# Optimization experiments

Hardware: AMD Instinct MI355X
Metric: run time of the kernel (lower is better)

## Reference

```python
import jax, jax.numpy as jnp
import numpy as np

N_EMBD = 512
N_HEADS = 8
N_KV_HEADS = 2
HEAD_DIM = N_EMBD // N_HEADS  # 64
ROPE_BASE = 1000000.0
B, T = 2, 4096


def _rotate_half(x):
    h = x.shape[-1] // 2
    return jnp.concatenate([-x[..., h:], x[..., :h]], axis=-1)


def _build_rope(head_dim, seq_len, base, dtype):
    inv_freq = 1.0 / base ** (jnp.arange(0, head_dim, 2, dtype=jnp.float32) / head_dim)
    t = jnp.arange(seq_len, dtype=jnp.float32)
    freqs = jnp.outer(t, inv_freq)            # [T, head_dim/2]
    emb = jnp.concatenate([freqs, freqs], axis=-1)  # [T, head_dim]
    return emb.astype(dtype), None  # placeholder, cos/sin computed by caller


def setup_inputs() -> dict:
    key = jax.random.key(0)
    ks = jax.random.split(key, 8)
    s_in = 1.0 / np.sqrt(N_EMBD)
    x = jax.random.normal(ks[0], (B, T, N_EMBD), dtype=jnp.float32)
    Wq = jax.random.normal(ks[1], (N_EMBD, N_HEADS * HEAD_DIM), dtype=jnp.float32) * s_in
    bq = jnp.zeros((N_HEADS * HEAD_DIM,), dtype=jnp.float32)
    Wk = jax.random.normal(ks[2], (N_EMBD, N_KV_HEADS * HEAD_DIM), dtype=jnp.float32) * s_in
    bk = jnp.zeros((N_KV_HEADS * HEAD_DIM,), dtype=jnp.float32)
    Wv = jax.random.normal(ks[3], (N_EMBD, N_KV_HEADS * HEAD_DIM), dtype=jnp.float32) * s_in
    bv = jnp.zeros((N_KV_HEADS * HEAD_DIM,), dtype=jnp.float32)
    Wo = jax.random.normal(ks[4], (N_HEADS * HEAD_DIM, N_EMBD), dtype=jnp.float32) * s_in
    return {"x": x, "Wq": Wq, "bq": bq, "Wk": Wk, "bk": bk, "Wv": Wv, "bv": bv, "Wo": Wo}


def reference(x, Wq, bq, Wk, bk, Wv, bv, Wo):
    Bx, Tx, _ = x.shape
    scale = HEAD_DIM ** -0.5
    q = (x @ Wq + bq).reshape(Bx, Tx, N_HEADS, HEAD_DIM).transpose(0, 2, 1, 3)      # [B,H,T,D]
    k = (x @ Wk + bk).reshape(Bx, Tx, N_KV_HEADS, HEAD_DIM).transpose(0, 2, 1, 3)   # [B,Hkv,T,D]
    v = (x @ Wv + bv).reshape(Bx, Tx, N_KV_HEADS, HEAD_DIM).transpose(0, 2, 1, 3)

    # RoPE (built in fp32 then cast, matching torch impl)
    inv_freq = 1.0 / ROPE_BASE ** (jnp.arange(0, HEAD_DIM, 2, dtype=jnp.float32) / HEAD_DIM)
    t = jnp.arange(Tx, dtype=jnp.float32)
    freqs = jnp.outer(t, inv_freq)
    emb = jnp.concatenate([freqs, freqs], axis=-1)          # [T, D]
    cos = jnp.cos(emb).astype(x.dtype)[None, None, :, :]    # broadcast over B,H
    sin = jnp.sin(emb).astype(x.dtype)[None, None, :, :]
    q = q * cos + _rotate_half(q) * sin
    k = k * cos + _rotate_half(k) * sin

    rep = N_HEADS // N_KV_HEADS
    k = jnp.repeat(k, rep, axis=1)   # repeat_interleave on head dim
    v = jnp.repeat(v, rep, axis=1)

    attn = jnp.einsum("bhtd,bhsd->bhts", q, k) * scale      # [B,H,T,T]
    causal = jnp.tril(jnp.ones((Tx, Tx), dtype=bool))
    attn = jnp.where(causal, attn, jnp.finfo(attn.dtype).min)
    attn = jax.nn.softmax(attn, axis=-1)
    out = jnp.einsum("bhts,bhsd->bhtd", attn, v)            # [B,H,T,D]
    out = out.transpose(0, 2, 1, 3).reshape(Bx, Tx, N_HEADS * HEAD_DIM)
    return out @ Wo
```

## Files before the change

kernel.cpp:

```cpp
#include <hip/hip_runtime.h>

typedef unsigned short u16;
typedef unsigned int u32;
typedef __bf16 bf16x8_t __attribute__((ext_vector_type(8)));
typedef float f32x4_t __attribute__((ext_vector_type(4)));
typedef float f32x16_t __attribute__((ext_vector_type(16)));

#define T_SEQ 4096
#define EMB 512
#define NH 8
#define NKV 2
#define HD 64

__device__ __forceinline__ float bf2f(u16 h) {
    union { unsigned u; float f; } x; x.u = ((unsigned)h) << 16; return x.f;
}
__device__ __forceinline__ u16 f2bf(float f) {
    union { float f; unsigned u; } x; x.f = f;
    unsigned r = x.u + 0x7FFFu + ((x.u >> 16) & 1u);
    return (u16)(r >> 16);
}

__global__ __launch_bounds__(256)
void prep_kernel(const float* __restrict__ x,
                 const float* __restrict__ Wq, const float* __restrict__ Wk,
                 const float* __restrict__ Wv, const float* __restrict__ Wo,
                 u16* __restrict__ WqkvT, u16* __restrict__ WoT,
                 u16* __restrict__ xbf, float* __restrict__ cost, float* __restrict__ sint)
{
    int i = blockIdx.x * 256 + threadIdx.x;
    if (i < 262144) {
        int n = i >> 9, k = i & 511;
        WqkvT[i] = f2bf(Wq[(size_t)k * 512 + n]);
    } else if (i < 327680) {
        int j = i - 262144;
        int n = j >> 9, k = j & 511;
        WqkvT[i] = f2bf(Wk[(size_t)k * 128 + n]);
    } else if (i < 393216) {
        int j = i - 327680;
        int n = j >> 9, k = j & 511;
        WqkvT[i] = f2bf(Wv[(size_t)k * 128 + n]);
    } else if (i < 655360) {
        int j = i - 393216;
        int n = j >> 9, k = j & 511;
        WoT[j] = f2bf(Wo[(size_t)k * 512 + n]);
    } else if (i < 1703936) {
        int j = i - 655360;
        float4 v = *reinterpret_cast<const float4*>(x + (size_t)j * 4);
        u16 o[4] = { f2bf(v.x), f2bf(v.y), f2bf(v.z), f2bf(v.w) };
        *reinterpret_cast<uint2*>(xbf + (size_t)j * 4) = *reinterpret_cast<uint2*>(o);
    } else {
        int j = i - 1703936;
        int t = j >> 5, jj = j & 31;
        double invf = pow(1.0e6, -(double)jj / 32.0);
        double ang = (double)t * invf;
        cost[j] = (float)cos(ang);
        sint[j] = (float)sin(ang);
    }
}

template <int EPI>
__global__ __launch_bounds__(256)
void gemm_kernel(const u16* __restrict__ A, const u16* __restrict__ Bt, int K,
                 float* __restrict__ C, int N,
                 const float* __restrict__ bq, const float* __restrict__ bk,
                 const float* __restrict__ bv,
                 const float* __restrict__ cost, const float* __restrict__ sint,
                 u16* __restrict__ qw, u16* __restrict__ kw, u16* __restrict__ vt)
{
    __shared__ __align__(16) u16 As[128][72];
    __shared__ __align__(16) u16 Bs[128][72];

    const int tid  = threadIdx.x;
    const int lane = tid & 63, wave = tid >> 6;
    const int wr = wave >> 1, wc = wave & 1;
    const int tm = blockIdx.x, tn = blockIdx.y;
    const int lrow = lane & 15, lgrp = lane >> 4;

    f32x4_t acc[4][4];
#pragma unroll
    for (int i = 0; i < 4; ++i)
#pragma unroll
        for (int j = 0; j < 4; ++j) acc[i][j] = (f32x4_t){0.f, 0.f, 0.f, 0.f};

    for (int k0 = 0; k0 < K; k0 += 64) {
        __syncthreads();
        {
            const int r0 = tid >> 3;
            const int ko = (tid & 7) * 8;
#pragma unroll
            for (int rr = 0; rr < 4; ++rr) {
                int row = r0 + rr * 32;
                uint4 va = *reinterpret_cast<const uint4*>(A + (size_t)(tm * 128 + row) * K + k0 + ko);
                *reinterpret_cast<uint4*>(&As[row][ko]) = va;
                uint4 vb = *reinterpret_cast<const uint4*>(Bt + (size_t)(tn * 128 + row) * K + k0 + ko);
                *reinterpret_cast<uint4*>(&Bs[row][ko]) = vb;
            }
        }
        __syncthreads();
#pragma unroll
        for (int kc = 0; kc < 2; ++kc) {
            bf16x8_t af[4], bf[4];
#pragma unroll
            for (int mb = 0; mb < 4; ++mb)
                af[mb] = *reinterpret_cast<const bf16x8_t*>(&As[wr * 64 + mb * 16 + lrow][kc * 32 + lgrp * 8]);
#pragma unroll
            for (int nb = 0; nb < 4; ++nb)
                bf[nb] = *reinterpret_cast<const bf16x8_t*>(&Bs[wc * 64 + nb * 16 + lrow][kc * 32 + lgrp * 8]);
#pragma unroll
            for (int mb = 0; mb < 4; ++mb)
#pragma unroll
                for (int nb = 0; nb < 4; ++nb)
                    acc[mb][nb] = __builtin_amdgcn_mfma_f32_16x16x32_bf16(af[mb], bf[nb], acc[mb][nb], 0, 0, 0);
        }
    }

    if (EPI == 0) {
#pragma unroll
        for (int mb = 0; mb < 4; ++mb)
#pragma unroll
            for (int nb = 0; nb < 4; ++nb)
#pragma unroll
                for (int r = 0; r < 4; ++r) {
                    int row = tm * 128 + wr * 64 + mb * 16 + lgrp * 4 + r;
                    int col = tn * 128 + wc * 64 + nb * 16 + lrow;
                    C[(size_t)row * N + col] = acc[mb][nb][r];
                }
    } else {
        const float QSC = 0.125f * 1.44269504088896f;
#pragma unroll
        for (int mb = 0; mb < 4; ++mb)
#pragma unroll
            for (int r = 0; r < 4; ++r) {
                int grow = tm * 128 + wr * 64 + mb * 16 + lgrp * 4 + r;
                int b = grow >> 12, t = grow & 4095;
#pragma unroll
                for (int nb = 0; nb < 2; ++nb) {
                    int n = tn * 128 + wc * 64 + nb * 16 + lrow;
                    int j = n & 63;
                    float c0 = acc[mb][nb][r];
                    float c1 = acc[mb][nb + 2][r];
                    if (n < 512) {
                        c0 += bq[n]; c1 += bq[n + 32];
                        float cs = cost[t * 32 + j], sn = sint[t * 32 + j];
                        float r0 = (c0 * cs - c1 * sn) * QSC;
                        float r1 = (c1 * cs + c0 * sn) * QSC;
                        int h = n >> 6;
                        size_t base = ((size_t)(b * NH + h) * T_SEQ + t) * HD;
                        qw[base + j]      = f2bf(r0);
                        qw[base + j + 32] = f2bf(r1);
                    } else if (n < 640) {
                        int nn = n - 512;
                        c0 += bk[nn]; c1 += bk[nn + 32];
                        float cs = cost[t * 32 + j], sn = sint[t * 32 + j];
                        float r0 = c0 * cs - c1 * sn;
                        float r1 = c1 * cs + c0 * sn;
                        int hk2 = nn >> 6;
                        size_t base = ((size_t)(b * NKV + hk2) * T_SEQ + t) * HD;
                        kw[base + j]      = f2bf(r0);
                        kw[base + j + 32] = f2bf(r1);
                    } else {
                        int nn = n - 640;
                        c0 += bv[nn]; c1 += bv[nn + 32];
                        int hv = nn >> 6;
                        size_t base = (size_t)(b * NKV + hv) * HD * T_SEQ;
                        vt[base + (size_t)j * T_SEQ + t]        = f2bf(c0);
                        vt[base + (size_t)(j + 32) * T_SEQ + t] = f2bf(c1);
                    }
                }
            }
    }
}

__global__ __launch_bounds__(256)
void attn_kernel(const u16* __restrict__ qw, const u16* __restrict__ kw,
                 const u16* __restrict__ vt, u16* __restrict__ po, float* __restrict__ lb)
{
    __shared__ __align__(16) u16 Ks[2][64][64];
    __shared__ __align__(16) u16 Vs[2][64][64];

    const int hdix = blockIdx.x;
    const int b = hdix >> 3, h = hdix & 7, hk = h >> 2;
    const int qt = 31 - (int)blockIdx.y;
    const int ck = blockIdx.z;
    const int tid = threadIdx.x, lane = tid & 63, wave = tid >> 6;
    const int lid = lane & 31, hi = lane >> 5;
    const int q0 = qt * 128 + wave * 32;
    const int kt0 = ck * (qt + 1);
    const int kt1 = kt0 + (qt + 1);

    const u16* kbase  = kw + (size_t)(b * NKV + hk) * T_SEQ * HD;
    const u16* vtbase = vt + (size_t)(b * NKV + hk) * HD * T_SEQ;

    const int ss = tid >> 3;
    const int sg = tid & 7;
    const int swz = (sg ^ (ss & 7)) << 3;

    bf16x8_t qf[4];
    {
        const u16* qrow = qw + ((size_t)(b * NH + h) * T_SEQ + q0 + lid) * HD + 8 * hi;
#pragma unroll
        for (int t = 0; t < 4; ++t)
            qf[t] = *reinterpret_cast<const bf16x8_t*>(qrow + 16 * t);
    }

    f32x16_t o0, o1, z16;
#pragma unroll
    for (int i = 0; i < 16; ++i) { o0[i] = 0.f; o1[i] = 0.f; z16[i] = 0.f; }
    const float M_FIX = 16.0f;
    float l = 0.f;

    {
        const int s2 = kt0 * 64;
        uint4 ka  = *reinterpret_cast<const uint4*>(kbase + (size_t)(s2 + ss) * HD + sg * 8);
        uint4 kb2 = *reinterpret_cast<const uint4*>(kbase + (size_t)(s2 + ss + 32) * HD + sg * 8);
        uint4 va  = *reinterpret_cast<const uint4*>(vtbase + (size_t)ss * T_SEQ + s2 + sg * 8);
        uint4 vb2 = *reinterpret_cast<const uint4*>(vtbase + (size_t)(ss + 32) * T_SEQ + s2 + sg * 8);
        *reinterpret_cast<uint4*>(&Ks[0][ss][swz]) = ka;
        *reinterpret_cast<uint4*>(&Ks[0][ss + 32][swz]) = kb2;
        *reinterpret_cast<uint4*>(&Vs[0][ss][swz]) = va;
        *reinterpret_cast<uint4*>(&Vs[0][ss + 32][swz]) = vb2;
    }
    __syncthreads();

    for (int kt = kt0; kt < kt1; ++kt) {
        const int cur = (kt - kt0) & 1, nxt = cur ^ 1;
        const bool pre = (kt + 1 < kt1);

        uint4 kr0, kr1, vr0, vr1;
        if (pre) {
            const int s2 = (kt + 1) * 64;
            kr0 = *reinterpret_cast<const uint4*>(kbase + (size_t)(s2 + ss) * HD + sg * 8);
            kr1 = *reinterpret_cast<const uint4*>(kbase + (size_t)(s2 + ss + 32) * HD + sg * 8);
            vr0 = *reinterpret_cast<const uint4*>(vtbase + (size_t)ss * T_SEQ + s2 + sg * 8);
            vr1 = *reinterpret_cast<const uint4*>(vtbase + (size_t)(ss + 32) * T_SEQ + s2 + sg * 8);
        }

        if (kt * 64 <= q0 + 31) {
            const bool full = (kt * 64 + 32 <= q0 + 31);
            const bool mreq = (kt * 64 + 63 > q0);

            f32x16_t s0, s1;
            __builtin_amdgcn_s_setprio(1);
#pragma unroll
            for (int t = 0; t < 4; ++t) {
                const int g = ((2 * t + hi) ^ (lid & 7)) << 3;
                bf16x8_t ka = *reinterpret_cast<const bf16x8_t*>(&Ks[cur][lid][g]);
                s0 = __builtin_amdgcn_mfma_f32_32x32x16_bf16(ka, qf[t], (t == 0) ? z16 : s0, 0, 0, 0);
                if (full) {
                    bf16x8_t kb2 = *reinterpret_cast<const bf16x8_t*>(&Ks[cur][lid + 32][g]);
                    s1 = __builtin_amdgcn_mfma_f32_32x32x16_bf16(kb2, qf[t], (t == 0) ? z16 : s1, 0, 0, 0);
                }
            }
            __builtin_amdgcn_s_setprio(0);

            if (mreq) {
                const int qg = q0 + lid;
                const int kvb = kt * 64 + 4 * hi;
#pragma unroll
                for (int r = 0; r < 16; ++r) {
                    int kv = kvb + (r & 3) + 8 * (r >> 2);
                    if (kv > qg) s0[r] = -1e30f;
                    if (full && kv + 32 > qg) s1[r] = -1e30f;
                }
            }

#pragma unroll
            for (int r = 0; r < 16; ++r) s0[r] = exp2f(s0[r] - M_FIX);
            if (full) {
#pragma unroll
                for (int r = 0; r < 16; ++r) s1[r] = exp2f(s1[r] - M_FIX);
            }

            {
                float rs = 0.f;
#pragma unroll
                for (int q4 = 0; q4 < 4; ++q4)
                    rs += (s0[4 * q4] + s0[4 * q4 + 1]) + (s0[4 * q4 + 2] + s0[4 * q4 + 3]);
                if (full) {
#pragma unroll
                    for (int q4 = 0; q4 < 4; ++q4)
                        rs += (s1[4 * q4] + s1[4 * q4 + 1]) + (s1[4 * q4 + 2] + s1[4 * q4 + 3]);
                }
                rs += __shfl_xor(rs, 32);
                l += rs;
            }

            bf16x8_t pa[4];
            {
                u32 pw[8];
#pragma unroll
                for (int c = 0; c < 4; ++c) {
                    asm("v_cvt_pk_bf16_f32 %0, %1, %2" : "=v"(pw[2 * c])     : "v"(s0[4 * c]),     "v"(s0[4 * c + 1]));
                    asm("v_cvt_pk_bf16_f32 %0, %1, %2" : "=v"(pw[2 * c + 1]) : "v"(s0[4 * c + 2]), "v"(s0[4 * c + 3]));
                }
                asm("v_permlane32_swap_b32 %0, %1" : "+v"(pw[0]), "+v"(pw[2]));
                asm("v_permlane32_swap_b32 %0, %1" : "+v"(pw[1]), "+v"(pw[3]));
                asm("v_permlane32_swap_b32 %0, %1" : "+v"(pw[4]), "+v"(pw[6]));
                asm("v_permlane32_swap_b32 %0, %1" : "+v"(pw[5]), "+v"(pw[7]));
                uint4 f0 = {pw[0], pw[1], pw[2], pw[3]};
                uint4 f1 = {pw[4], pw[5], pw[6], pw[7]};
                pa[0] = __builtin_bit_cast(bf16x8_t, f0);
                pa[1] = __builtin_bit_cast(bf16x8_t, f1);
                if (full) {
#pragma unroll
                    for (int c = 0; c < 4; ++c) {
                        asm("v_cvt_pk_bf16_f32 %0, %1, %2" : "=v"(pw[2 * c])     : "v"(s1[4 * c]),     "v"(s1[4 * c + 1]));
                        asm("v_cvt_pk_bf16_f32 %0, %1, %2" : "=v"(pw[2 * c + 1]) : "v"(s1[4 * c + 2]), "v"(s1[4 * c + 3]));
                    }
                    asm("v_permlane32_swap_b32 %0, %1" : "+v"(pw[0]), "+v"(pw[2]));
                    asm("v_permlane32_swap_b32 %0, %1" : "+v"(pw[1]), "+v"(pw[3]));
                    asm("v_permlane32_swap_b32 %0, %1" : "+v"(pw[4]), "+v"(pw[6]));
                    asm("v_permlane32_swap_b32 %0, %1" : "+v"(pw[5]), "+v"(pw[7]));
                    uint4 g0 = {pw[0], pw[1], pw[2], pw[3]};
                    uint4 g1 = {pw[4], pw[5], pw[6], pw[7]};
                    pa[2] = __builtin_bit_cast(bf16x8_t, g0);
                    pa[3] = __builtin_bit_cast(bf16x8_t, g1);
                }
            }

            __builtin_amdgcn_s_setprio(1);
            const int ns = full ? 4 : 2;
#pragma unroll
            for (int s = 0; s < 4; ++s) {
                if (s >= ns) break;
                const int g = ((2 * s + hi) ^ (lid & 7)) << 3;
                bf16x8_t v0f = *reinterpret_cast<const bf16x8_t*>(&Vs[cur][lid][g]);
                bf16x8_t v1f = *reinterpret_cast<const bf16x8_t*>(&Vs[cur][lid + 32][g]);
                o0 = __builtin_amdgcn_mfma_f32_32x32x16_bf16(pa[s], v0f, o0, 0, 0, 0);
                o1 = __builtin_amdgcn_mfma_f32_32x32x16_bf16(pa[s], v1f, o1, 0, 0, 0);
            }
            __builtin_amdgcn_s_setprio(0);
        }

        if (pre) {
            *reinterpret_cast<uint4*>(&Ks[nxt][ss][swz]) = kr0;
            *reinterpret_cast<uint4*>(&Ks[nxt][ss + 32][swz]) = kr1;
            *reinterpret_cast<uint4*>(&Vs[nxt][ss][swz]) = vr0;
            *reinterpret_cast<uint4*>(&Vs[nxt][ss + 32][swz]) = vr1;
            __syncthreads();
        }
    }

    {
        u16* pob = po + (size_t)ck * 4194304;
        const int rowb = (hdix * 32 + qt) * 128;
#pragma unroll
        for (int r = 0; r < 16; ++r) {
            int qr = (r & 3) + 8 * (r >> 2) + 4 * hi;
            size_t base = (size_t)(rowb + wave * 32 + qr) * HD;
            pob[base + lid]      = f2bf(o0[r]);
            pob[base + lid + 32] = f2bf(o1[r]);
        }
        if (hi == 0)
            lb[(size_t)ck * 65536 + rowb + wave * 32 + lid] = l;
    }
}

__global__ __launch_bounds__(256)
void combine_kernel(const u16* __restrict__ po, const float* __restrict__ lb,
                    u16* __restrict__ ao)
{
    int id = blockIdx.x * 256 + threadIdx.x;
    int row = id >> 3, oct = id & 7;
    int bhqt = row >> 7, qrow = row & 127;
    int bh = bhqt >> 5, qt = bhqt & 31;
    int b = bh >> 3, h = bh & 7;
    int t = qt * 128 + qrow;

    float inv = 1.0f / (lb[row] + lb[65536 + row]);
    const u16* p0 = po + (size_t)row * HD + oct * 8;
    const u16* p1 = p0 + 4194304;
    uint4 a = *reinterpret_cast<const uint4*>(p0);
    uint4 c = *reinterpret_cast<const uint4*>(p1);
    const u16* pa = reinterpret_cast<const u16*>(&a);
    const u16* pc = reinterpret_cast<const u16*>(&c);
    u16 outv[8];
#pragma unroll
    for (int j = 0; j < 8; ++j)
        outv[j] = f2bf((bf2f(pa[j]) + bf2f(pc[j])) * inv);
    size_t base = ((size_t)(b * T_SEQ) + t) * EMB + h * HD + oct * 8;
    *reinterpret_cast<uint2*>(ao + base)     = *reinterpret_cast<uint2*>(&outv[0]);
    *reinterpret_cast<uint2*>(ao + base + 4) = *reinterpret_cast<uint2*>(&outv[4]);
}

extern "C" void kernel_launch(void* const* d_in, const int* in_sizes, int n_in,
                              void* d_out, int out_size, void* d_ws, size_t ws_size,
                              hipStream_t stream)
{
    const float* x  = (const float*)d_in[0];
    const float* Wq = (const float*)d_in[1];
    const float* bq = (const float*)d_in[2];
    const float* Wk = (const float*)d_in[3];
    const float* bk = (const float*)d_in[4];
    const float* Wv = (const float*)d_in[5];
    const float* bv = (const float*)d_in[6];
    const float* Wo = (const float*)d_in[7];
    float* out = (float*)d_out;

    char* ws = (char*)d_ws;
    u16*   WqkvT = (u16*)(ws);
    u16*   WoT   = (u16*)(ws + 786432);
    float* cost  = (float*)(ws + 1310720);
    float* sint  = (float*)(ws + 1835008);
    u16*   xbf   = (u16*)(ws + 2359296);
    u16*   qw    = (u16*)(ws + 10747904);
    u16*   kw    = (u16*)(ws + 19136512);
    u16*   vt    = (u16*)(ws + 21233664);
    u16*   ao    = (u16*)(ws + 23330816);
    u16*   po    = (u16*)(ws + 31719424);
    float* lb    = (float*)(ws + 48496640);

    prep_kernel<<<7168, 256, 0, stream>>>(x, Wq, Wk, Wv, Wo, WqkvT, WoT, xbf, cost, sint);

    dim3 gp(64, 6);
    gemm_kernel<1><<<gp, 256, 0, stream>>>(xbf, WqkvT, 512, nullptr, 768,
                                           bq, bk, bv, cost, sint, qw, kw, vt);

    dim3 ga(2 * NH, 32, 2);
    attn_kernel<<<ga, 256, 0, stream>>>(qw, kw, vt, po, lb);

    combine_kernel<<<65536 * 8 / 256, 256, 0, stream>>>(po, lb, ao);

    dim3 go(64, 4);
    gemm_kernel<0><<<go, 256, 0, stream>>>(ao, WoT, 512, out, 512,
                                           nullptr, nullptr, nullptr, nullptr, nullptr,
                                           nullptr, nullptr, nullptr);
}
```

Baseline: 134.3 us.

## Fuse x bf16 conversion and split-K combine into GEMM A-tile loads

Removes the separate fp32-to-bf16 conversion of x from the prep kernel by converting on the fly while loading A tiles in the QKV GEMM. Removes the combine kernel by merging the two attention partial outputs and normalizing by the summed l values inside the output-projection GEMM's A-tile load. This saves a kernel launch and the round trips of the xbf and ao intermediates through global memory. In exchange, the A-load path does more global reads and ALU work, and the recombination is repeated for each N-tile column block (4x).

```diff
diff --git a/kernel.cpp b/kernel.cpp
--- a/kernel.cpp
+++ b/kernel.cpp
@@ -22,11 +22,10 @@
 }
 
 __global__ __launch_bounds__(256)
-void prep_kernel(const float* __restrict__ x,
-                 const float* __restrict__ Wq, const float* __restrict__ Wk,
+void prep_kernel(const float* __restrict__ Wq, const float* __restrict__ Wk,
                  const float* __restrict__ Wv, const float* __restrict__ Wo,
                  u16* __restrict__ WqkvT, u16* __restrict__ WoT,
-                 u16* __restrict__ xbf, float* __restrict__ cost, float* __restrict__ sint)
+                 float* __restrict__ cost, float* __restrict__ sint)
 {
     int i = blockIdx.x * 256 + threadIdx.x;
     if (i < 262144) {
@@ -44,13 +43,8 @@
         int j = i - 393216;
         int n = j >> 9, k = j & 511;
         WoT[j] = f2bf(Wo[(size_t)k * 512 + n]);
-    } else if (i < 1703936) {
+    } else {
         int j = i - 655360;
-        float4 v = *reinterpret_cast<const float4*>(x + (size_t)j * 4);
-        u16 o[4] = { f2bf(v.x), f2bf(v.y), f2bf(v.z), f2bf(v.w) };
-        *reinterpret_cast<uint2*>(xbf + (size_t)j * 4) = *reinterpret_cast<uint2*>(o);
-    } else {
-        int j = i - 1703936;
         int t = j >> 5, jj = j & 31;
         double invf = pow(1.0e6, -(double)jj / 32.0);
         double ang = (double)t * invf;
@@ -59,9 +53,11 @@
     }
 }
 
-template <int EPI>
+template <int EPI, int ASRC>
 __global__ __launch_bounds__(256)
-void gemm_kernel(const u16* __restrict__ A, const u16* __restrict__ Bt, int K,
+void gemm_kernel(const u16* __restrict__ A, const float* __restrict__ Af32,
+                 const u16* __restrict__ po1, const float* __restrict__ lbp,
+                 const u16* __restrict__ Bt, int K,
                  float* __restrict__ C, int N,
                  const float* __restrict__ bq, const float* __restrict__ bk,
                  const float* __restrict__ bv,
@@ -91,8 +87,31 @@
 #pragma unroll
             for (int rr = 0; rr < 4; ++rr) {
                 int row = r0 + rr * 32;
-                uint4 va = *reinterpret_cast<const uint4*>(A + (size_t)(tm * 128 + row) * K + k0 + ko);
-                *reinterpret_cast<uint4*>(&As[row][ko]) = va;
+                int grow = tm * 128 + row;
+                if (ASRC == 0) {
+                    uint4 va = *reinterpret_cast<const uint4*>(A + (size_t)grow * K + k0 + ko);
+                    *reinterpret_cast<uint4*>(&As[row][ko]) = va;
+                } else if (ASRC == 1) {
+                    float4 f0 = *reinterpret_cast<const float4*>(Af32 + (size_t)grow * K + k0 + ko);
+                    float4 f1 = *reinterpret_cast<const float4*>(Af32 + (size_t)grow * K + k0 + ko + 4);
+                    u16 o[8] = { f2bf(f0.x), f2bf(f0.y), f2bf(f0.z), f2bf(f0.w),
+                                 f2bf(f1.x), f2bf(f1.y), f2bf(f1.z), f2bf(f1.w) };
+                    *reinterpret_cast<uint4*>(&As[row][ko]) = *reinterpret_cast<uint4*>(o);
+                } else {
+                    int b2 = grow >> 12, t2 = grow & 4095;
+                    int h2 = k0 >> 6;
+                    size_t prow = (size_t)(b2 * 8 + h2) * 4096 + t2;
+                    float inv = 1.0f / (lbp[prow] + lbp[65536 + prow]);
+                    uint4 a = *reinterpret_cast<const uint4*>(A   + prow * 64 + ko);
+                    uint4 c = *reinterpret_cast<const uint4*>(po1 + prow * 64 + ko);
+                    const u16* pa = reinterpret_cast<const u16*>(&a);
+                    const u16* pc = reinterpret_cast<const u16*>(&c);
+                    u16 o[8];
+#pragma unroll
+                    for (int j = 0; j < 8; ++j)
+                        o[j] = f2bf((bf2f(pa[j]) + bf2f(pc[j])) * inv);
+                    *reinterpret_cast<uint4*>(&As[row][ko]) = *reinterpret_cast<uint4*>(o);
+                }
                 uint4 vb = *reinterpret_cast<const uint4*>(Bt + (size_t)(tn * 128 + row) * K + k0 + ko);
                 *reinterpret_cast<uint4*>(&Bs[row][ko]) = vb;
             }
@@ -357,33 +376,6 @@
     }
 }
 
-__global__ __launch_bounds__(256)
-void combine_kernel(const u16* __restrict__ po, const float* __restrict__ lb,
-                    u16* __restrict__ ao)
-{
-    int id = blockIdx.x * 256 + threadIdx.x;
-    int row = id >> 3, oct = id & 7;
-    int bhqt = row >> 7, qrow = row & 127;
-    int bh = bhqt >> 5, qt = bhqt & 31;
-    int b = bh >> 3, h = bh & 7;
-    int t = qt * 128 + qrow;
-
-    float inv = 1.0f / (lb[row] + lb[65536 + row]);
-    const u16* p0 = po + (size_t)row * HD + oct * 8;
-    const u16* p1 = p0 + 4194304;
-    uint4 a = *reinterpret_cast<const uint4*>(p0);
-    uint4 c = *reinterpret_cast<const uint4*>(p1);
-    const u16* pa = reinterpret_cast<const u16*>(&a);
-    const u16* pc = reinterpret_cast<const u16*>(&c);
-    u16 outv[8];
-#pragma unroll
-    for (int j = 0; j < 8; ++j)
-        outv[j] = f2bf((bf2f(pa[j]) + bf2f(pc[j])) * inv);
-    size_t base = ((size_t)(b * T_SEQ) + t) * EMB + h * HD + oct * 8;
-    *reinterpret_cast<uint2*>(ao + base)     = *reinterpret_cast<uint2*>(&outv[0]);
-    *reinterpret_cast<uint2*>(ao + base + 4) = *reinterpret_cast<uint2*>(&outv[4]);
-}
-
 extern "C" void kernel_launch(void* const* d_in, const int* in_sizes, int n_in,
                               void* d_out, int out_size, void* d_ws, size_t ws_size,
                               hipStream_t stream)
@@ -403,27 +395,25 @@
     u16*   WoT   = (u16*)(ws + 786432);
     float* cost  = (float*)(ws + 1310720);
     float* sint  = (float*)(ws + 1835008);
-    u16*   xbf   = (u16*)(ws + 2359296);
     u16*   qw    = (u16*)(ws + 10747904);
     u16*   kw    = (u16*)(ws + 19136512);
     u16*   vt    = (u16*)(ws + 21233664);
-    u16*   ao    = (u16*)(ws + 23330816);
     u16*   po    = (u16*)(ws + 31719424);
     float* lb    = (float*)(ws + 48496640);
 
-    prep_kernel<<<7168, 256, 0, stream>>>(x, Wq, Wk, Wv, Wo, WqkvT, WoT, xbf, cost, sint);
+    prep_kernel<<<3072, 256, 0, stream>>>(Wq, Wk, Wv, Wo, WqkvT, WoT, cost, sint);
 
     dim3 gp(64, 6);
-    gemm_kernel<1><<<gp, 256, 0, stream>>>(xbf, WqkvT, 512, nullptr, 768,
-                                           bq, bk, bv, cost, sint, qw, kw, vt);
+    gemm_kernel<1, 1><<<gp, 256, 0, stream>>>(nullptr, x, nullptr, nullptr, WqkvT, 512,
+                                              nullptr, 768,
+                                              bq, bk, bv, cost, sint, qw, kw, vt);
 
     dim3 ga(2 * NH, 32, 2);
     attn_kernel<<<ga, 256, 0, stream>>>(qw, kw, vt, po, lb);
 
-    combine_kernel<<<65536 * 8 / 256, 256, 0, stream>>>(po, lb, ao);
-
     dim3 go(64, 4);
-    gemm_kernel<0><<<go, 256, 0, stream>>>(ao, WoT, 512, out, 512,
-                                           nullptr, nullptr, nullptr, nullptr, nullptr,
-                                           nullptr, nullptr, nullptr);
-}
+    gemm_kernel<0, 2><<<go, 256, 0, stream>>>(po, nullptr, po + 4194304, lb, WoT, 512,
+                                              out, 512,
+                                              nullptr, nullptr, nullptr, nullptr, nullptr,
+                                              nullptr, nullptr, nullptr);
+}
```

Result: no change. 137.0 us (+2.0%).
